# Performance work log

Measured on AMD Instinct MI355X. Metric: run time of the kernel, lower is better.

The kernel has to match this reference:

```python
import jax, jax.numpy as jnp
import numpy as np

NB, CH, NY, NX, NC = 2, 64, 80, 80, 80
STRIDE = 4.0


def _conv(x, w, b, pad):
    y = jax.lax.conv_general_dilated(x, w, (1, 1), [(pad, pad), (pad, pad)],
                                     dimension_numbers=('NCHW', 'OIHW', 'NCHW'))
    return y + b[None, :, None, None]


def _head(x, w1, b1, w2, b2, final_relu):
    y = jax.nn.relu(_conv(x, w1, b1, 1))
    y = _conv(y, w2, b2, 0)
    return jax.nn.relu(y) if final_relu else y


def setup_inputs() -> dict:
    key = jax.random.key(0)
    ks = jax.random.split(key, 16)
    s = 0.05

    def cw(k, o, i, kk):
        return jax.random.normal(k, (o, i, kk, kk), jnp.float32) * s

    def cb(k, o):
        return jax.random.normal(k, (o,), jnp.float32) * s

    inp = {
        'x': jax.random.normal(ks[0], (NB, CH, NY, NX), jnp.float32),
        # offsets: [batch_index, off_x, off_y] per image (esod tile offsets)
        'offsets': jnp.concatenate([
            jnp.arange(NB, dtype=jnp.float32)[:, None],
            jax.random.uniform(ks[1], (NB, 2), jnp.float32) * 4.0], axis=1),
        'hm_w1': cw(ks[2], CH, CH, 3), 'hm_b1': cb(ks[3], CH),
        'hm_w2': cw(ks[4], NC, CH, 1), 'hm_b2': jnp.full((NC,), -2.19, jnp.float32),
        'wh_w1': cw(ks[5], CH, CH, 3), 'wh_b1': cb(ks[6], CH),
        'wh_w2': cw(ks[7], 2, CH, 1), 'wh_b2': cb(ks[8], 2),
        'reg_w1': cw(ks[9], CH, CH, 3), 'reg_b1': cb(ks[10], CH),
        'reg_w2': cw(ks[11], 2, CH, 1), 'reg_b2': cb(ks[12], 2),
    }
    return inp


def _forward(x, offsets, hm_w1, hm_b1, hm_w2, hm_b2,
             wh_w1, wh_b1, wh_w2, wh_b2,
             reg_w1, reg_b1, reg_w2, reg_b2):
    hm = _head(x, hm_w1, hm_b1, hm_w2, hm_b2, False)    # (nb, nc, ny, nx)
    wh = _head(x, wh_w1, wh_b1, wh_w2, wh_b2, True)     # (nb, 2, ny, nx)
    reg = _head(x, reg_w1, reg_b1, reg_w2, reg_b2, True)
    nb, nc, ny, nx = hm.shape

    wh_ = jnp.transpose(wh, (0, 2, 3, 1))   # (nb, ny, nx, 2)
    reg_ = jnp.transpose(reg, (0, 2, 3, 1))
    yv, xv = jnp.meshgrid(jnp.arange(ny), jnp.arange(nx), indexing='ij')
    grid = jnp.stack([xv, yv], -1).astype(jnp.float32)[None]  # (1, ny, nx, 2)

    off_xy = offsets[:, 1:3].reshape(nb, 1, 1, 2) * 2.0
    ctr = grid + off_xy + reg_
    bbox = jnp.concatenate([ctr - wh_ / 2.0, ctr + wh_ / 2.0], -1) * STRIDE  # xyxy

    # xyxy -> xywh (same per-image boxes for every class channel)
    cxy = (bbox[..., :2] + bbox[..., 2:]) / 2.0
    bwh = bbox[..., 2:] - bbox[..., :2]
    xywh = jnp.concatenate([cxy, bwh], -1)              # (nb, ny, nx, 4)

    hm_ = jax.nn.sigmoid(hm)
    hmax = jax.lax.reduce_window(hm_, -jnp.inf, jax.lax.max,
                                 (1, 1, 3, 3), (1, 1, 1, 1),
                                 [(0, 0), (0, 0), (1, 1), (1, 1)])
    maxima = (hmax == hm_)                              # (nb, nc, ny, nx)

    no = 5 + nc
    xywh_b = jnp.broadcast_to(xywh[:, None], (nb, nc, ny, nx, 4))
    score = hm_[..., None]
    oh = jnp.broadcast_to(jnp.eye(nc, dtype=hm_.dtype)[None, :, None, None, :],
                          (nb, nc, ny, nx, nc))
    rows = jnp.concatenate([xywh_b, score, oh], -1)     # (nb, nc, ny, nx, no)

    K = nc * ny * nx
    rows = rows.reshape(nb, K, no)
    m = maxima.reshape(nb, K)

    def compact(r, mk):
        # stable sort: maxima rows first, preserving (c, y, x) scan order
        order = jnp.argsort(jnp.logical_not(mk), stable=True)
        return r[order] * mk[order][:, None].astype(r.dtype)

    return jax.vmap(compact)(rows, m)                   # (nb, K, 5+nc), zero-padded


def reference(x, offsets, hm_w1, hm_b1, hm_w2, hm_b2,
              wh_w1, wh_b1, wh_w2, wh_b2,
              reg_w1, reg_b1, reg_w2, reg_b2):
    return _forward(x, offsets, hm_w1, hm_b1, hm_w2, hm_b2,
                    wh_w1, wh_b1, wh_w2, wh_b2,
                    reg_w1, reg_b1, reg_w2, reg_b2)
```

## Files before the change

### kernel.cpp

```cpp
#include <hip/hip_runtime.h>
#include <math.h>

#define NBATCH 2
#define CHN    64
#define NYY    80
#define NXX    80
#define NCLS   80
#define NPIX   6400
#define KTOT   512000
#define NOUT   85
#define NBLK   500

typedef float vf4 __attribute__((ext_vector_type(4)));

#define QTOT   21760000L
#define QF1    11980800L
#define QF2    15257600L
#define QF3    20377600L

__global__ __launch_bounds__(320)
void conv1_kernel(const float* __restrict__ x,
                  const float* __restrict__ hw1, const float* __restrict__ hb1,
                  const float* __restrict__ ww1, const float* __restrict__ wb1,
                  const float* __restrict__ rw1, const float* __restrict__ rb1,
                  double* __restrict__ c1hm, float* __restrict__ c1wr,
                  vf4* __restrict__ outq)
{
    __shared__ double smem_d[6144];
    const int bl = blockIdx.x;
    const int t  = threadIdx.x;

    const int gtid = bl * 320 + t;
    const int nth  = 480 * 320;
    const vf4 fz = {0.f, 0.f, 0.f, 0.f};

    const int pxq = t % 80;
    const int ocq = t / 80;
    const int r   = pxq / 20;
    const int c   = (pxq % 20) * 4;

    float* lxf = (float*)smem_d;

    if (bl % 3 == 0) {
        double* lwd = (double*)((char*)smem_d + 30720);

        const int idx = bl / 3;
        const int yt  = idx % 20;
        const int ocg = (idx / 20) % 4;
        const int b   = idx / 80;
        const int oc0 = ocg * 16 + ocq * 4;
        const int gy0 = yt * 4;

        const float* xin = x + (size_t)b * CHN * NPIX;

        double acc[4][4];
        #pragma unroll
        for (int j = 0; j < 4; j++)
            #pragma unroll
            for (int o = 0; o < 4; o++) acc[j][o] = (double)hb1[oc0 + o];

        for (int cc = 0; cc < 4; cc++) {
            const int icc = cc * 16;
            __syncthreads();
            for (int j = t; j < 1920; j += 320) {
                int ic_l = j / 120; int rem = j % 120;
                int row_l = rem / 20; int c4 = (rem % 20) * 4;
                int gy = gy0 - 1 + row_l;
                float4 v = make_float4(0.f, 0.f, 0.f, 0.f);
                if ((unsigned)gy < 80u)
                    v = *(const float4*)(xin + (size_t)(icc + ic_l) * NPIX + gy * NXX + c4);
                *(float4*)&lxf[(ic_l * 6 + row_l) * 80 + c4] = v;
            }
            for (int j = t; j < 2304; j += 320) {
                int oc_l = j % 16; int k = j / 16;
                int ic_l = k / 9, tap = k % 9;
                lwd[k * 16 + oc_l] =
                    (double)hw1[((size_t)(ocg * 16 + oc_l) * CHN + icc + ic_l) * 9 + tap];
            }
            __syncthreads();
            {
                int i0 = cc * 20, i1 = (cc == 3) ? 78 : cc * 20 + 20;
                for (int i = i0; i < i1; i++) {
                    long q = (long)gtid + (long)i * nth;
                    if (q < QF1) __builtin_nontemporal_store(fz, outq + q);
                }
            }
            for (int ic = 0; ic < 16; ic++) {
                double xw[3][6];
                #pragma unroll
                for (int ky = 0; ky < 3; ky++) {
                    const float* row = &lxf[(ic * 6 + r + ky) * 80];
                    xw[ky][0] = (c > 0) ? (double)row[c - 1] : 0.0;
                    float4 m = *(const float4*)&row[c];
                    xw[ky][1] = (double)m.x; xw[ky][2] = (double)m.y;
                    xw[ky][3] = (double)m.z; xw[ky][4] = (double)m.w;
                    xw[ky][5] = (c < 76) ? (double)row[c + 4] : 0.0;
                }
                #pragma unroll
                for (int ky = 0; ky < 3; ky++)
                #pragma unroll
                for (int kx = 0; kx < 3; kx++) {
                    const double* wv = &lwd[(ic * 9 + ky * 3 + kx) * 16 + ocq * 4];
                    double w0 = wv[0], w1d = wv[1], w2 = wv[2], w3 = wv[3];
                    #pragma unroll
                    for (int j = 0; j < 4; j++) {
                        double xv = xw[ky][j + kx];
                        acc[j][0] += xv * w0; acc[j][1] += xv * w1d;
                        acc[j][2] += xv * w2; acc[j][3] += xv * w3;
                    }
                }
            }
        }
        size_t pix = (size_t)(gy0 + r) * NXX + c;
        #pragma unroll
        for (int o = 0; o < 4; o++) {
            double* dst = c1hm + ((size_t)b * CHN + oc0 + o) * NPIX + pix;
            double2 lo, hi;
            lo.x = acc[0][o] > 0.0 ? acc[0][o] : 0.0;
            lo.y = acc[1][o] > 0.0 ? acc[1][o] : 0.0;
            hi.x = acc[2][o] > 0.0 ? acc[2][o] : 0.0;
            hi.y = acc[3][o] > 0.0 ? acc[3][o] : 0.0;
            *(double2*)dst = lo;
            *(double2*)(dst + 2) = hi;
        }
    } else {
        float* lwf = (float*)((char*)smem_d + 30720);

        const int idx = bl - bl / 3 - 1;
        const int yt  = idx % 20;
        const int ocg = (idx / 20) % 4;
        const int img = idx / 80;

        const int head = img >> 1, b = img & 1;
        const float* w1 = (head == 0) ? ww1 : rw1;
        const float* b1 = (head == 0) ? wb1 : rb1;
        const float* xin = x + (size_t)b * CHN * NPIX;

        const int oc0 = ocg * 16 + ocq * 4;
        const int gy0 = yt * 4;

        float acc[4][4];
        #pragma unroll
        for (int j = 0; j < 4; j++)
            #pragma unroll
            for (int o = 0; o < 4; o++) acc[j][o] = b1[oc0 + o];

        for (int cc = 0; cc < 4; cc++) {
            const int icc = cc * 16;
            __syncthreads();
            for (int j = t; j < 1920; j += 320) {
                int ic_l = j / 120; int rem = j % 120;
                int row_l = rem / 20; int c4 = (rem % 20) * 4;
                int gy = gy0 - 1 + row_l;
                float4 v = make_float4(0.f, 0.f, 0.f, 0.f);
                if ((unsigned)gy < 80u)
                    v = *(const float4*)(xin + (size_t)(icc + ic_l) * NPIX + gy * NXX + c4);
                *(float4*)&lxf[(ic_l * 6 + row_l) * 80 + c4] = v;
            }
            for (int j = t; j < 2304; j += 320) {
                int oc_l = j % 16; int k = j / 16;
                int ic_l = k / 9, tap = k % 9;
                lwf[k * 16 + oc_l] =
                    w1[((size_t)(ocg * 16 + oc_l) * CHN + icc + ic_l) * 9 + tap];
            }
            __syncthreads();
            {
                int i0 = cc * 20, i1 = (cc == 3) ? 78 : cc * 20 + 20;
                for (int i = i0; i < i1; i++) {
                    long q = (long)gtid + (long)i * nth;
                    if (q < QF1) __builtin_nontemporal_store(fz, outq + q);
                }
            }
            for (int ic = 0; ic < 16; ic++) {
                float xw[3][6];
                #pragma unroll
                for (int ky = 0; ky < 3; ky++) {
                    const float* row = &lxf[(ic * 6 + r + ky) * 80];
                    xw[ky][0] = (c > 0) ? row[c - 1] : 0.f;
                    float4 m = *(const float4*)&row[c];
                    xw[ky][1] = m.x; xw[ky][2] = m.y;
                    xw[ky][3] = m.z; xw[ky][4] = m.w;
                    xw[ky][5] = (c < 76) ? row[c + 4] : 0.f;
                }
                #pragma unroll
                for (int ky = 0; ky < 3; ky++)
                #pragma unroll
                for (int kx = 0; kx < 3; kx++) {
                    const float* wv = &lwf[(ic * 9 + ky * 3 + kx) * 16 + ocq * 4];
                    float w0 = wv[0], w1v = wv[1], w2 = wv[2], w3 = wv[3];
                    #pragma unroll
                    for (int j = 0; j < 4; j++) {
                        float xv = xw[ky][j + kx];
                        acc[j][0] += xv * w0; acc[j][1] += xv * w1v;
                        acc[j][2] += xv * w2; acc[j][3] += xv * w3;
                    }
                }
            }
        }
        size_t pix = (size_t)(gy0 + r) * NXX + c;
        #pragma unroll
        for (int o = 0; o < 4; o++) {
            float4 v;
            v.x = fmaxf(acc[0][o], 0.f); v.y = fmaxf(acc[1][o], 0.f);
            v.z = fmaxf(acc[2][o], 0.f); v.w = fmaxf(acc[3][o], 0.f);
            *(float4*)(c1wr + ((size_t)img * CHN + oc0 + o) * NPIX + pix) = v;
        }
    }
}

__global__ __launch_bounds__(256)
void conv2_kernel(const double* __restrict__ c1hm,
                  const float* __restrict__ hm_w2, const float* __restrict__ hm_b2,
                  const float* __restrict__ c1wr,
                  const float* __restrict__ wh_w2, const float* __restrict__ wh_b2,
                  const float* __restrict__ rg_w2, const float* __restrict__ rg_b2,
                  double* __restrict__ hm_z, float* __restrict__ wh, float* __restrict__ rg,
                  vf4* __restrict__ outq)
{
    __shared__ double smem2[9216];
    const int bl = blockIdx.x;
    const int t  = threadIdx.x;

    {
        const int gtid = bl * 256 + t;
        const vf4 fz = {0.f, 0.f, 0.f, 0.f};
        for (int i = 0; i < 32; i++) {
            long q = QF1 + (long)gtid + (long)i * 102400;
            if (q < QF2) __builtin_nontemporal_store(fz, outq + q);
        }
    }

    if (bl < 200) {
        double* lx = smem2;
        double* lw = smem2 + 4096;

        const int b   = bl / 100;
        const int px0 = (bl % 100) * 64;

        const double* in = c1hm + (size_t)b * CHN * NPIX;
        for (int j = t; j < 4096; j += 256) {
            int ic = j >> 6, px = j & 63;
            lx[j] = in[(size_t)ic * NPIX + px0 + px];
        }
        for (int j = t; j < 5120; j += 256) {
            int ic = j / 80, oc = j % 80;
            lw[j] = (double)hm_w2[(size_t)oc * CHN + ic];
        }
        __syncthreads();

        const int px  = t & 63;
        const int ocg = t >> 6;
        double acc[20];
        #pragma unroll
        for (int o = 0; o < 20; o++) acc[o] = (double)hm_b2[ocg * 20 + o];

        for (int ic = 0; ic < 64; ic++) {
            double xv = lx[ic * 64 + px];
            const double* wrow = &lw[ic * 80 + ocg * 20];
            #pragma unroll
            for (int o = 0; o < 20; o++) acc[o] += xv * wrow[o];
        }
        #pragma unroll
        for (int o = 0; o < 20; o++)
            hm_z[((size_t)b * NCLS + ocg * 20 + o) * NPIX + px0 + px] = acc[o];
    } else {
        const int blw  = bl - 200;
        const int chunk = blw % 25;
        const int hc   = (blw / 25) % 4;
        const int b    = blw / 100;
        const int head = hc >> 1, ch = hc & 1;

        const int p = chunk * 256 + t;
        const float* in = c1wr + ((size_t)(head * 2 + b) * CHN) * NPIX;
        const float* w  = (head == 0) ? wh_w2 + (size_t)ch * CHN : rg_w2 + (size_t)ch * CHN;
        float acc = (head == 0) ? wh_b2[ch] : rg_b2[ch];
        for (int ic = 0; ic < CHN; ic++) acc += in[(size_t)ic * NPIX + p] * w[ic];
        acc = fmaxf(acc, 0.f);
        float* o = (head == 0) ? wh : rg;
        o[((size_t)b * 2 + ch) * NPIX + p] = acc;
    }
}

__global__ void flags_kernel(const double* __restrict__ hm_z,
                             unsigned long long* __restrict__ ballots,
                             unsigned int* __restrict__ counts,
                             vf4* __restrict__ outq)
{
    int b = blockIdx.y;
    int k = blockIdx.x * 1024 + threadIdx.x;

    {
        const int gtid = (b * NBLK + blockIdx.x) * 1024 + threadIdx.x;
        const vf4 fz = {0.f, 0.f, 0.f, 0.f};
        for (int i = 0; i < 5; i++) {
            long q = QF2 + (long)gtid + (long)i * 1024000;
            if (q < QF3) __builtin_nontemporal_store(fz, outq + q);
        }
    }

    int c = k / NPIX;
    int p = k - c * NPIX;
    int y = p / NXX, xx = p - y * NXX;

    const double* h = hm_z + ((size_t)b * NCLS + c) * NPIX;
    double s = h[p];
    double m = s;
    #pragma unroll
    for (int dy = -1; dy <= 1; dy++) {
        int yy = y + dy;
        if ((unsigned)yy >= (unsigned)NYY) continue;
        const double* hr = h + yy * NXX;
        #pragma unroll
        for (int dx = -1; dx <= 1; dx++) {
            int xn = xx + dx;
            if ((unsigned)xn >= (unsigned)NXX) continue;
            double v = hr[xn];
            m = v > m ? v : m;
        }
    }
    bool flag = (s == m);
    unsigned long long ball = __ballot(flag);
    int lane = threadIdx.x & 63;
    int wave = threadIdx.x >> 6;

    __shared__ unsigned int wcnt[16];
    if (lane == 0) {
        ballots[(size_t)b * 8000 + blockIdx.x * 16 + wave] = ball;
        wcnt[wave] = __popcll(ball);
    }
    __syncthreads();
    if (threadIdx.x == 0) {
        unsigned int tot = 0;
        for (int i = 0; i < 16; i++) tot += wcnt[i];
        counts[b * NBLK + blockIdx.x] = tot;
    }
}

__global__ void scan_kernel(const unsigned int* __restrict__ counts,
                            unsigned int* __restrict__ offs)
{
    int b = blockIdx.x;
    int t = threadIdx.x;
    unsigned int v = (t < NBLK) ? counts[b * NBLK + t] : 0u;
    unsigned int xi = v;
    #pragma unroll
    for (int d = 1; d < 64; d <<= 1) {
        unsigned int n = __shfl_up(xi, d, 64);
        if ((t & 63) >= d) xi += n;
    }
    __shared__ unsigned int wtot[8];
    __shared__ unsigned int wbase[8];
    if ((t & 63) == 63) wtot[t >> 6] = xi;
    __syncthreads();
    if (t == 0) {
        unsigned int a = 0;
        for (int i = 0; i < 8; i++) { wbase[i] = a; a += wtot[i]; }
    }
    __syncthreads();
    unsigned int excl = xi - v + wbase[t >> 6];
    if (t < NBLK) offs[b * NBLK + t] = excl;
}

__global__ void scatter_kernel(const unsigned long long* __restrict__ ballots,
                               const unsigned int* __restrict__ offs,
                               const double* __restrict__ hm_z,
                               const float* __restrict__ wh,
                               const float* __restrict__ rg,
                               const float* __restrict__ offsets,
                               float* __restrict__ out,
                               vf4* __restrict__ outq)
{
    int b = blockIdx.y;
    int k = blockIdx.x * 1024 + threadIdx.x;
    int lane = threadIdx.x & 63;
    int wave = threadIdx.x >> 6;

    {
        const int gtid = (b * NBLK + blockIdx.x) * 1024 + threadIdx.x;
        const vf4 fz = {0.f, 0.f, 0.f, 0.f};
        for (int i = 0; i < 2; i++) {
            long q = QF3 + (long)gtid + (long)i * 1024000;
            if (q < QTOT) __builtin_nontemporal_store(fz, outq + q);
        }
    }

    unsigned long long ball = ballots[(size_t)b * 8000 + blockIdx.x * 16 + wave];

    __shared__ unsigned int wc[16];
    __shared__ unsigned int wb[16];
    if (lane == 0) wc[wave] = __popcll(ball);
    __syncthreads();
    if (threadIdx.x == 0) {
        unsigned int a = 0;
        for (int i = 0; i < 16; i++) { wb[i] = a; a += wc[i]; }
    }
    __syncthreads();

    bool flag = (ball >> lane) & 1ull;
    if (!flag) return;

    unsigned int rank = offs[b * NBLK + blockIdx.x] + wb[wave]
                      + (unsigned int)__popcll(ball & ((1ull << lane) - 1ull));

    int c = k / NPIX;
    int p = k - c * NPIX;
    int y = p / NXX, xx = p - y * NXX;

    float offx = offsets[b * 3 + 1];
    float offy = offsets[b * 3 + 2];
    float r0 = rg[((size_t)b * 2 + 0) * NPIX + p];
    float r1 = rg[((size_t)b * 2 + 1) * NPIX + p];
    float w0 = wh[((size_t)b * 2 + 0) * NPIX + p];
    float w1 = wh[((size_t)b * 2 + 1) * NPIX + p];
    double z = hm_z[((size_t)b * NCLS + c) * NPIX + p];
    float s  = (float)(1.0 / (1.0 + exp(-z)));

    float cx = ((float)xx + 2.f * offx + r0) * 4.f;
    float cy = ((float)y  + 2.f * offy + r1) * 4.f;

    float* row = out + ((size_t)b * KTOT + rank) * NOUT;
    row[0] = cx;
    row[1] = cy;
    row[2] = w0 * 4.f;
    row[3] = w1 * 4.f;
    row[4] = s;
    row[5 + c] = 1.f;
}

extern "C" void kernel_launch(void* const* d_in, const int* in_sizes, int n_in,
                              void* d_out, int out_size, void* d_ws, size_t ws_size,
                              hipStream_t stream)
{
    const float* x       = (const float*)d_in[0];
    const float* offsets = (const float*)d_in[1];
    const float* hm_w1   = (const float*)d_in[2];
    const float* hm_b1   = (const float*)d_in[3];
    const float* hm_w2   = (const float*)d_in[4];
    const float* hm_b2   = (const float*)d_in[5];
    const float* wh_w1   = (const float*)d_in[6];
    const float* wh_b1   = (const float*)d_in[7];
    const float* wh_w2   = (const float*)d_in[8];
    const float* wh_b2   = (const float*)d_in[9];
    const float* reg_w1  = (const float*)d_in[10];
    const float* reg_b1  = (const float*)d_in[11];
    const float* reg_w2  = (const float*)d_in[12];
    const float* reg_b2  = (const float*)d_in[13];

    float* out = (float*)d_out;
    vf4* outq  = (vf4*)d_out;

    char* wp = (char*)d_ws;
    double* c1hm = (double*)wp;                 wp += (size_t)NBATCH * CHN * NPIX * 8;
    double* hm_z = (double*)wp;                 wp += (size_t)NBATCH * NCLS * NPIX * 8;
    float*  c1wr = (float*)wp;                  wp += (size_t)2 * NBATCH * CHN * NPIX * 4;
    float*  wh   = (float*)wp;                  wp += (size_t)NBATCH * 2 * NPIX * 4;
    float*  rg   = (float*)wp;                  wp += (size_t)NBATCH * 2 * NPIX * 4;
    unsigned long long* ballots = (unsigned long long*)wp; wp += (size_t)NBATCH * 8000 * 8;
    unsigned int* counts = (unsigned int*)wp;   wp += (size_t)NBATCH * NBLK * 4;
    unsigned int* offs   = (unsigned int*)wp;

    conv1_kernel<<<480, 320, 0, stream>>>(
        x, hm_w1, hm_b1, wh_w1, wh_b1, reg_w1, reg_b1, c1hm, c1wr, outq);

    conv2_kernel<<<400, 256, 0, stream>>>(
        c1hm, hm_w2, hm_b2, c1wr, wh_w2, wh_b2, reg_w2, reg_b2,
        hm_z, wh, rg, outq);

    flags_kernel<<<dim3(NBLK, 2), 1024, 0, stream>>>(hm_z, ballots, counts, outq);

    scan_kernel<<<2, 512, 0, stream>>>(counts, offs);

    scatter_kernel<<<dim3(NBLK, 2), 1024, 0, stream>>>(
        ballots, offs, hm_z, wh, rg, offsets, out, outq);
}
```

Before: 151.8 us.

## Fold prefix scan into scatter and rebalance output zero-fill across kernels

Removes the separate scan kernel; each scatter block now sums the preceding block counts itself with a wave reduction to find its base rank. The zero-fill of the output is redistributed so conv1, conv2 and flags cover it entirely and scatter no longer writes zeros. This saves a kernel launch and the scatter-side fill, at the cost of redundant per-block count summation and more fill work in earlier kernels.

```diff
diff --git a/kernel.cpp b/kernel.cpp
--- a/kernel.cpp
+++ b/kernel.cpp
@@ -14,9 +14,8 @@
 typedef float vf4 __attribute__((ext_vector_type(4)));
 
 #define QTOT   21760000L
-#define QF1    11980800L
-#define QF2    15257600L
-#define QF3    20377600L
+#define QF1    14131200L
+#define QF2    18534400L
 
 __global__ __launch_bounds__(320)
 void conv1_kernel(const float* __restrict__ x,
@@ -79,7 +78,7 @@
             }
             __syncthreads();
             {
-                int i0 = cc * 20, i1 = (cc == 3) ? 78 : cc * 20 + 20;
+                int i0 = cc * 23, i1 = i0 + 23;
                 for (int i = i0; i < i1; i++) {
                     long q = (long)gtid + (long)i * nth;
                     if (q < QF1) __builtin_nontemporal_store(fz, outq + q);
@@ -165,7 +164,7 @@
             }
             __syncthreads();
             {
-                int i0 = cc * 20, i1 = (cc == 3) ? 78 : cc * 20 + 20;
+                int i0 = cc * 23, i1 = i0 + 23;
                 for (int i = i0; i < i1; i++) {
                     long q = (long)gtid + (long)i * nth;
                     if (q < QF1) __builtin_nontemporal_store(fz, outq + q);
@@ -224,7 +223,7 @@
     {
         const int gtid = bl * 256 + t;
         const vf4 fz = {0.f, 0.f, 0.f, 0.f};
-        for (int i = 0; i < 32; i++) {
+        for (int i = 0; i < 43; i++) {
             long q = QF1 + (long)gtid + (long)i * 102400;
             if (q < QF2) __builtin_nontemporal_store(fz, outq + q);
         }
@@ -292,9 +291,9 @@
     {
         const int gtid = (b * NBLK + blockIdx.x) * 1024 + threadIdx.x;
         const vf4 fz = {0.f, 0.f, 0.f, 0.f};
-        for (int i = 0; i < 5; i++) {
+        for (int i = 0; i < 4; i++) {
             long q = QF2 + (long)gtid + (long)i * 1024000;
-            if (q < QF3) __builtin_nontemporal_store(fz, outq + q);
+            if (q < QTOT) __builtin_nontemporal_store(fz, outq + q);
         }
     }
 
@@ -336,72 +335,51 @@
     }
 }
 
-__global__ void scan_kernel(const unsigned int* __restrict__ counts,
-                            unsigned int* __restrict__ offs)
-{
-    int b = blockIdx.x;
-    int t = threadIdx.x;
-    unsigned int v = (t < NBLK) ? counts[b * NBLK + t] : 0u;
-    unsigned int xi = v;
-    #pragma unroll
-    for (int d = 1; d < 64; d <<= 1) {
-        unsigned int n = __shfl_up(xi, d, 64);
-        if ((t & 63) >= d) xi += n;
-    }
-    __shared__ unsigned int wtot[8];
-    __shared__ unsigned int wbase[8];
-    if ((t & 63) == 63) wtot[t >> 6] = xi;
-    __syncthreads();
-    if (t == 0) {
-        unsigned int a = 0;
-        for (int i = 0; i < 8; i++) { wbase[i] = a; a += wtot[i]; }
-    }
-    __syncthreads();
-    unsigned int excl = xi - v + wbase[t >> 6];
-    if (t < NBLK) offs[b * NBLK + t] = excl;
-}
-
 __global__ void scatter_kernel(const unsigned long long* __restrict__ ballots,
-                               const unsigned int* __restrict__ offs,
+                               const unsigned int* __restrict__ counts,
                                const double* __restrict__ hm_z,
                                const float* __restrict__ wh,
                                const float* __restrict__ rg,
                                const float* __restrict__ offsets,
-                               float* __restrict__ out,
-                               vf4* __restrict__ outq)
+                               float* __restrict__ out)
 {
-    int b = blockIdx.y;
-    int k = blockIdx.x * 1024 + threadIdx.x;
-    int lane = threadIdx.x & 63;
-    int wave = threadIdx.x >> 6;
-
-    {
-        const int gtid = (b * NBLK + blockIdx.x) * 1024 + threadIdx.x;
-        const vf4 fz = {0.f, 0.f, 0.f, 0.f};
-        for (int i = 0; i < 2; i++) {
-            long q = QF3 + (long)gtid + (long)i * 1024000;
-            if (q < QTOT) __builtin_nontemporal_store(fz, outq + q);
-        }
-    }
-
-    unsigned long long ball = ballots[(size_t)b * 8000 + blockIdx.x * 16 + wave];
-
+    __shared__ unsigned int csum[512];
     __shared__ unsigned int wc[16];
     __shared__ unsigned int wb[16];
+    __shared__ unsigned int sbase;
+
+    int b  = blockIdx.y;
+    int bx = blockIdx.x;
+    int t  = threadIdx.x;
+    int lane = t & 63;
+    int wave = t >> 6;
+
+    if (t < 512) csum[t] = (t < NBLK) ? counts[b * NBLK + t] : 0u;
+
+    unsigned long long ball = ballots[(size_t)b * 8000 + bx * 16 + wave];
     if (lane == 0) wc[wave] = __popcll(ball);
     __syncthreads();
-    if (threadIdx.x == 0) {
-        unsigned int a = 0;
-        for (int i = 0; i < 16; i++) { wb[i] = a; a += wc[i]; }
+
+    if (t < 64) {
+        unsigned int s = 0;
+        for (int j = t; j < bx; j += 64) s += csum[j];
+        #pragma unroll
+        for (int d = 32; d >= 1; d >>= 1) s += __shfl_xor(s, d, 64);
+        if (t == 0) {
+            sbase = s;
+            unsigned int a = 0;
+            for (int i = 0; i < 16; i++) { wb[i] = a; a += wc[i]; }
+        }
     }
     __syncthreads();
 
     bool flag = (ball >> lane) & 1ull;
     if (!flag) return;
 
-    unsigned int rank = offs[b * NBLK + blockIdx.x] + wb[wave]
+    unsigned int rank = sbase + wb[wave]
                       + (unsigned int)__popcll(ball & ((1ull << lane) - 1ull));
 
+    int k = bx * 1024 + t;
     int c = k / NPIX;
     int p = k - c * NPIX;
     int y = p / NXX, xx = p - y * NXX;
@@ -456,8 +434,7 @@
     float*  wh   = (float*)wp;                  wp += (size_t)NBATCH * 2 * NPIX * 4;
     float*  rg   = (float*)wp;                  wp += (size_t)NBATCH * 2 * NPIX * 4;
     unsigned long long* ballots = (unsigned long long*)wp; wp += (size_t)NBATCH * 8000 * 8;
-    unsigned int* counts = (unsigned int*)wp;   wp += (size_t)NBATCH * NBLK * 4;
-    unsigned int* offs   = (unsigned int*)wp;
+    unsigned int* counts = (unsigned int*)wp;
 
     conv1_kernel<<<480, 320, 0, stream>>>(
         x, hm_w1, hm_b1, wh_w1, wh_b1, reg_w1, reg_b1, c1hm, c1wr, outq);
@@ -468,8 +445,6 @@
 
     flags_kernel<<<dim3(NBLK, 2), 1024, 0, stream>>>(hm_z, ballots, counts, outq);
 
-    scan_kernel<<<2, 512, 0, stream>>>(counts, offs);
-
     scatter_kernel<<<dim3(NBLK, 2), 1024, 0, stream>>>(
-        ballots, offs, hm_z, wh, rg, offsets, out, outq);
+        ballots, counts, hm_z, wh, rg, offsets, out);
 }
```

New measurement: 148.5 us. 2.2% less time.
